# Optimization experiments

Hardware: AMD Instinct MI355X
Metric: run time of the kernel (lower is better)

## Reference

```python
import jax, jax.numpy as jnp
import numpy as np

B, S, D = 2, 2048, 4096
H, KVH, HD = 32, 8, 128
MULT = 0.08838834764831845  # 1/sqrt(head_dim)
MAXV = 30.0                 # tanh soft-cap
ROPE_BASE = 10000.0


def _rope_cos_sin(position_ids, hd=HD, base=ROPE_BASE):
    inv_freq = 1.0 / (base ** (jnp.arange(0, hd, 2, dtype=jnp.float32) / hd))
    freqs = position_ids.astype(jnp.float32)[..., None] * inv_freq  # [B,S,hd/2]
    emb = jnp.concatenate([freqs, freqs], axis=-1)                  # [B,S,hd]
    return jnp.cos(emb), jnp.sin(emb)


def _rotate_half(x):
    half = x.shape[-1] // 2
    return jnp.concatenate([-x[..., half:], x[..., :half]], axis=-1)


def setup_inputs() -> dict:
    key = jax.random.key(0)
    ks = jax.random.split(key, 5)
    hidden_states = jax.random.normal(ks[0], (B, S, D), dtype=jnp.float32)
    position_ids = jnp.broadcast_to(jnp.arange(S, dtype=jnp.int64), (B, S))
    # True = masked (causal upper triangle)
    causal = jnp.triu(jnp.ones((S, S), dtype=bool), k=1)
    attention_mask = jnp.broadcast_to(causal, (B, 1, S, S))
    sc = 0.02
    q_w = jax.random.normal(ks[1], (D, H * HD), dtype=jnp.float32) * sc
    k_w = jax.random.normal(ks[2], (D, KVH * HD), dtype=jnp.float32) * sc
    v_w = jax.random.normal(ks[3], (D, KVH * HD), dtype=jnp.float32) * sc
    o_w = jax.random.normal(ks[4], (H * HD, D), dtype=jnp.float32) * sc
    return {"hidden_states": hidden_states, "position_ids": position_ids,
            "attention_mask": attention_mask, "q_w": q_w, "k_w": k_w,
            "v_w": v_w, "o_w": o_w}


def reference(hidden_states, position_ids, attention_mask, q_w, k_w, v_w, o_w):
    bsz, q_len, _ = hidden_states.shape
    q = (hidden_states @ q_w).reshape(bsz, q_len, H, HD).transpose(0, 2, 1, 3)    # [B,H,S,HD]
    k = (hidden_states @ k_w).reshape(bsz, q_len, KVH, HD).transpose(0, 2, 1, 3)  # [B,KVH,S,HD]
    v = (hidden_states @ v_w).reshape(bsz, q_len, KVH, HD).transpose(0, 2, 1, 3)

    cos, sin = _rope_cos_sin(position_ids)   # [B,S,HD]
    cos = cos[:, None]                       # [B,1,S,HD]
    sin = sin[:, None]
    q = q * cos + _rotate_half(q) * sin
    k = k * cos + _rotate_half(k) * sin

    groups = H // KVH
    k = jnp.repeat(k, groups, axis=1)        # [B,H,S,HD]
    v = jnp.repeat(v, groups, axis=1)

    scores = jnp.einsum('bhqd,bhkd->bhqk', q, k).astype(jnp.float32) * MULT
    scores = MAXV * jnp.tanh(scores / MAXV)
    scores = jnp.where(attention_mask, jnp.float32(-10000.0), scores)
    attn = jax.nn.softmax(scores, axis=-1).astype(q.dtype)

    out = jnp.einsum('bhqk,bhkd->bhqd', attn, v)       # [B,H,S,HD]
    out = out.transpose(0, 2, 1, 3).reshape(bsz, q_len, H * HD)
    return out @ o_w
```

## Files before the change

kernel.cpp:

```cpp
#include <hip/hip_runtime.h>
#include <stdint.h>

#define B_ 2
#define S_ 2048
#define D_ 4096
#define H_ 32
#define KVH_ 8
#define HD_ 128
#define GRP_ (H_/KVH_)
#define NQKV 6144
#define MULT_ 0.08838834764831845f
#define MAXV_ 30.0f

typedef __attribute__((ext_vector_type(8))) short s16x8;
typedef __attribute__((ext_vector_type(4))) float fx4;

__device__ __forceinline__ unsigned short f2bf(float f) {
  unsigned int u = __float_as_uint(f);
  u += 0x7fffu + ((u >> 16) & 1u);
  return (unsigned short)(u >> 16);
}
__device__ __forceinline__ float bf2f(unsigned short h) {
  return __uint_as_float(((unsigned int)h) << 16);
}

__device__ __forceinline__ void gld_lds16(const void* g, void* l) {
  __builtin_amdgcn_global_load_lds(
      (const __attribute__((address_space(1))) unsigned int*)g,
      (__attribute__((address_space(3))) unsigned int*)l, 16, 0, 0);
}


__global__ void k_f2bf(const float* __restrict__ src, unsigned short* __restrict__ dst, int n4) {
  int i = blockIdx.x * blockDim.x + threadIdx.x;
  int stride = gridDim.x * blockDim.x;
  for (; i < n4; i += stride) {
    float4 v = ((const float4*)src)[i];
    ushort4 o;
    o.x = f2bf(v.x); o.y = f2bf(v.y); o.z = f2bf(v.z); o.w = f2bf(v.w);
    ((ushort4*)dst)[i] = o;
  }
}

__global__ void k_transpose_w(const float* __restrict__ src, int ncols,
                              unsigned short* __restrict__ dst) {
  __shared__ float tile[32][33];
  int k0 = blockIdx.x * 32;
  int n0 = blockIdx.y * 32;
  int tx = threadIdx.x, ty = threadIdx.y;
  for (int i = 0; i < 32; i += 8)
    tile[ty + i][tx] = src[(size_t)(k0 + ty + i) * ncols + n0 + tx];
  __syncthreads();
  for (int i = 0; i < 32; i += 8)
    dst[(size_t)(n0 + ty + i) * 4096 + k0 + tx] = f2bf(tile[tx][ty + i]);
}

__global__ void k_transpose_v(const unsigned short* __restrict__ qkv,
                              unsigned short* __restrict__ vt) {
  __shared__ unsigned short tile[32][33];
  int s0 = blockIdx.x * 32;
  int d0 = blockIdx.y * 32;
  int bk = blockIdx.z;
  int b = bk / KVH_, kvh = bk % KVH_;
  int tx = threadIdx.x, ty = threadIdx.y;
  for (int i = 0; i < 32; i += 8)
    tile[ty + i][tx] = qkv[(size_t)(b*S_ + s0 + ty + i)*NQKV + 5120 + kvh*HD_ + d0 + tx];
  __syncthreads();
  for (int i = 0; i < 32; i += 8)
    vt[((size_t)bk*HD_ + d0 + ty + i)*S_ + s0 + tx] = tile[tx][ty + i];
}

__global__ void k_rope(const unsigned short* __restrict__ qkv,
                       unsigned short* __restrict__ Q, unsigned short* __restrict__ K) {
  int bs = blockIdx.x;
  int b = bs >> 11;
  int s = bs & (S_ - 1);
  __shared__ float cs[64], sn[64];
  int t = threadIdx.x;
  if (t < 64) {
    float inv = __expf(-(float)t * 0.14391156831212787f);
    float fr = (float)s * inv;
    cs[t] = cosf(fr); sn[t] = sinf(fr);
  }
  __syncthreads();
  const unsigned short* row = qkv + (size_t)bs * NQKV;
  for (int i = t; i < H_*HD_; i += 256) {
    int h = i >> 7, d = i & 127;
    float x = bf2f(row[i]);
    float x2, c, si;
    if (d < 64) { x2 = -bf2f(row[h*128 + d + 64]); c = cs[d];    si = sn[d]; }
    else        { x2 =  bf2f(row[h*128 + d - 64]); c = cs[d-64]; si = sn[d-64]; }
    Q[((size_t)(b*H_ + h)*S_ + s)*HD_ + d] = f2bf(x*c + x2*si);
  }
  for (int i = t; i < KVH_*HD_; i += 256) {
    int h = i >> 7, d = i & 127;
    float x = bf2f(row[4096 + i]);
    float x2, c, si;
    if (d < 64) { x2 = -bf2f(row[4096 + h*128 + d + 64]); c = cs[d];    si = sn[d]; }
    else        { x2 =  bf2f(row[4096 + h*128 + d - 64]); c = cs[d-64]; si = sn[d-64]; }
    K[((size_t)(b*KVH_ + h)*S_ + s)*HD_ + d] = f2bf(x*c + x2*si);
  }
}


#define BAR() asm volatile("s_barrier" ::: "memory")
#define SB0() __builtin_amdgcn_sched_barrier(0)

#define STAGE(buf, isB, h, kt) do {                                          \
  const unsigned short* _src = (isB) ? Bt : A;                               \
  size_t _rb = (size_t)(((isB) ? bn : bm)*((isB) ? BN : 256)                 \
                        + (h)*((isB) ? BN/2 : 128));                         \
  _Pragma("unroll") for (int _rr = 0; _rr < ((isB) ? BN/128 : 2); ++_rr) {   \
    int _s = _rr*8 + wv;                                                     \
    gld_lds16(_src + (_rb + (size_t)((_s>>1)*16))*Kd                         \
                   + (size_t)((kt)*64 + (_s&1)*32) + lane_off,               \
              ldsc + (buf)*PBUF + (isB)*32768                                \
                   + (h)*((isB) ? BN*64 : 16384) + _s*1024);                 \
  }                                                                          \
} while (0)

#define LDA(dst, buf, mh) do {                                               \
  _Pragma("unroll") for (int _i = 0; _i < 4; ++_i)                           \
  _Pragma("unroll") for (int _kk = 0; _kk < 2; ++_kk)                        \
    dst[_i*2+_kk] = *(const s16x8*)(ldsc + (buf)*PBUF + wr*16384             \
                    + ((((mh)*4+_i)*2+_kk)*1024) + aswz);                    \
} while (0)

#define LDB(dst, buf, nh) do {                                               \
  _Pragma("unroll") for (int _j = 0; _j < NFR; ++_j)                         \
  _Pragma("unroll") for (int _kk = 0; _kk < 2; ++_kk)                        \
    dst[_j*2+_kk] = *(const s16x8*)(ldsc + (buf)*PBUF + 32768                \
                    + (wc>>1)*(BN*64)                                        \
                    + ((((wc&1)*2*NFR+(nh)*NFR+_j)*2+_kk)*1024) + aswz);     \
} while (0)

#define MFMA_Q(Aa, Bb, MH, NH) do {                                          \
  __builtin_amdgcn_s_setprio(1);                                            \
  _Pragma("unroll") for (int _i = 0; _i < 4; ++_i)                           \
  _Pragma("unroll") for (int _j = 0; _j < NFR; ++_j)                         \
  _Pragma("unroll") for (int _kk = 0; _kk < 2; ++_kk)                        \
    acc[(MH)*4+_i][(NH)*NFR+_j] = __builtin_amdgcn_mfma_f32_16x16x32_bf16(   \
        Aa[_i*2+_kk], Bb[_j*2+_kk], acc[(MH)*4+_i][(NH)*NFR+_j], 0, 0, 0);   \
  __builtin_amdgcn_s_setprio(0);                                            \
} while (0)

template<int OUTF32, int BN>
__global__ __launch_bounds__(512, 2)
void k_gemm8(const unsigned short* __restrict__ A, const unsigned short* __restrict__ Bt,
             void* __restrict__ C, int Kdim, int N, int MB) {
  constexpr int NFR = BN / 128;
  constexpr int PBUF = 32768 + BN * 128;
  __shared__ __align__(16) char ldsbuf[2 * PBUF];
  char* ldsc = ldsbuf;
  const size_t Kd = (size_t)Kdim;
  const int NT = Kdim >> 6;

  auto VMCN = [] {
    if constexpr (BN == 256) asm volatile("s_waitcnt vmcnt(4)" ::: "memory");
    else                     asm volatile("s_waitcnt vmcnt(2)" ::: "memory");
  };

  int nwg = gridDim.x;
  int flat = blockIdx.x;
  int q = nwg >> 3, r8 = nwg & 7, xcd = flat & 7, off = flat >> 3;
  int wg = (xcd < r8 ? xcd*(q+1) : r8*(q+1) + (xcd-r8)*q) + off;
  int bm = wg % MB, bn = wg / MB;

  int tid = threadIdx.x;
  int lane = tid & 63, wv = tid >> 6;
  int wr = wv >> 2, wc = wv & 3;
  int l15 = lane & 15, l4 = lane >> 4;
  const int aswz = (l15 << 6) + ((l4 << 4) ^ ((l15 & 8) ? 32 : 0));
  const size_t lane_off = (size_t)(lane >> 2) * Kd
                        + (size_t)(((lane & 3) << 3) ^ ((lane & 32) >> 1));

  fx4 acc[8][2*NFR] = {};
  s16x8 Afr[8], B0fr[2*NFR], B1fr[2*NFR];

  STAGE(0, 0, 0, 0); STAGE(0, 0, 1, 0);
  STAGE(0, 1, 0, 0); STAGE(0, 1, 1, 0);
  STAGE(1, 1, 0, 1); STAGE(1, 1, 1, 1);
  VMCN();
  BAR();

  for (int t2 = 0; t2 < NT; t2 += 2) {
    int tb1 = t2 + 1;
    int tn0 = t2 + 2; if (tn0 >= NT) tn0 -= NT;
    int tn1 = t2 + 3; if (tn1 >= NT) tn1 -= NT;
    LDA(Afr, 0, 0); LDB(B0fr, 0, 0);
    STAGE(1, 0, 0, tb1);
    BAR();
    MFMA_Q(Afr, B0fr, 0, 0);
    SB0(); BAR();
    LDB(B1fr, 0, 1);
    STAGE(1, 0, 1, tb1);
    BAR();
    MFMA_Q(Afr, B1fr, 0, 1);
    SB0(); BAR();
    LDA(Afr, 0, 1);
    STAGE(0, 1, 0, tn0);
    BAR();
    MFMA_Q(Afr, B1fr, 1, 1);
    SB0(); BAR();
    STAGE(0, 1, 1, tn0);
    BAR();
    MFMA_Q(Afr, B0fr, 1, 0);
    SB0(); VMCN(); BAR();
    LDA(Afr, 1, 0); LDB(B0fr, 1, 0);
    STAGE(0, 0, 0, tn0);
    BAR();
    MFMA_Q(Afr, B0fr, 0, 0);
    SB0(); BAR();
    LDB(B1fr, 1, 1);
    STAGE(0, 0, 1, tn0);
    BAR();
    MFMA_Q(Afr, B1fr, 0, 1);
    SB0(); BAR();
    LDA(Afr, 1, 1);
    STAGE(1, 1, 0, tn1);
    BAR();
    MFMA_Q(Afr, B1fr, 1, 1);
    SB0(); BAR();
    STAGE(1, 1, 1, tn1);
    BAR();
    MFMA_Q(Afr, B0fr, 1, 0);
    SB0(); VMCN(); BAR();
  }

  int m0 = bm*256 + wr*128 + l4*4;
#pragma unroll
  for (int mf = 0; mf < 8; ++mf)
#pragma unroll
    for (int nf = 0; nf < 2*NFR; ++nf)
#pragma unroll
      for (int r = 0; r < 4; ++r) {
        int m = m0 + mf*16 + r;
        int n = bn*BN + (wc>>1)*(BN/2) + ((wc&1)*2*NFR + nf)*16 + l15;
        float v = acc[mf][nf][r];
        if (OUTF32) ((float*)C)[(size_t)m*N + n] = v;
        else ((unsigned short*)C)[(size_t)m*N + n] = f2bf(v);
      }
}


__global__ __launch_bounds__(256)
void k_attn7(const unsigned short* __restrict__ Q, const unsigned short* __restrict__ K,
             const unsigned short* __restrict__ Vt, unsigned short* __restrict__ Aout) {
  __shared__ unsigned short k_lds[2][32*128];
  __shared__ unsigned short v_lds[2][128*32];
  const float C1 = 0.08838834764831845f * 2.0f * 1.4426950408889634f / 30.0f;
  const float C2 = 30.0f * 1.4426950408889634f;
  int strip = 15 - blockIdx.x;
  int bh = blockIdx.y;
  int b = bh >> 5, h = bh & 31;
  int kvh = h >> 2;
  int tid = threadIdx.x, lane = tid & 63, wv = tid >> 6;
  int l15 = lane & 15, l4 = lane >> 4;
  const unsigned short* Qb = Q + (size_t)bh * S_ * HD_;
  const unsigned short* Kb = K + (size_t)(b*KVH_ + kvh) * S_ * HD_;
  const unsigned short* Vb = Vt + (size_t)(b*KVH_ + kvh) * HD_ * S_;

  int q0 = strip * 128;
  int qbase = q0 + wv * 32;
  s16x8 bq[2][4];
#pragma unroll
  for (int qf = 0; qf < 2; ++qf)
#pragma unroll
    for (int kb = 0; kb < 4; ++kb)
      bq[qf][kb] = *(const s16x8*)&Qb[(size_t)(qbase + qf*16 + l15)*HD_ + kb*32 + l4*8];

  s16x8 ones;
#pragma unroll
  for (int i = 0; i < 8; ++i) ones[i] = (short)0x3F80;

  fx4 oacc[2][8] = {};
  fx4 osum[2] = {};

  int nt_full = qbase >> 5;
  int nt_blk = strip*4 + 4;

#define STAGE_KV32(bufi, kb32) do {                                          \
  _Pragma("unroll") for (int _it = 0; _it < 2; ++_it) {                      \
    int _c = _it*256 + tid;                                                  \
    int _kr = _c >> 4;                                                       \
    int _kd = ((_c & 15) ^ (_kr & 7)) * 8;                                   \
    gld_lds16(&Kb[(size_t)((kb32) + _kr)*HD_ + _kd],                         \
              &k_lds[bufi][_it*2048 + wv*512]);                              \
    int _vd = _c >> 2;                                                       \
    int _vk = ((_c & 3) ^ (_vd & 3)) * 8;                                    \
    gld_lds16(&Vb[(size_t)_vd*S_ + (kb32) + _vk],                            \
              &v_lds[bufi][_it*2048 + wv*512]);                              \
  }                                                                          \
} while (0)

  auto body = [&](int bufi, int kbase, bool domask) {
    fx4 sst[2][2] = {};
    __builtin_amdgcn_s_setprio(1);
#pragma unroll
    for (int nb = 0; nb < 2; ++nb)
#pragma unroll
      for (int kb = 0; kb < 4; ++kb) {
        s16x8 kf = *(const s16x8*)&k_lds[bufi][(nb*16 + l15)*128 + (((kb*4 + l4) ^ (l15 & 7)) * 8)];
        sst[nb][0] = __builtin_amdgcn_mfma_f32_16x16x32_bf16(kf, bq[0][kb], sst[nb][0], 0, 0, 0);
        sst[nb][1] = __builtin_amdgcn_mfma_f32_16x16x32_bf16(kf, bq[1][kb], sst[nb][1], 0, 0, 0);
      }
    __builtin_amdgcn_s_setprio(0);
    s16x8 pf[2];
#pragma unroll
    for (int qf = 0; qf < 2; ++qf) {
      int qr = qbase + qf*16 + l15;
      uint32_t w[4];
#pragma unroll
      for (int nb = 0; nb < 2; ++nb) {
        float pv[4];
#pragma unroll
        for (int r = 0; r < 4; ++r) {
          float sraw = sst[nb][qf][r];
          float e2 = __builtin_amdgcn_exp2f(-fabsf(sraw) * C1);
          float th = (1.f - e2) * __builtin_amdgcn_rcpf(1.f + e2);
          float th_s = __uint_as_float(__float_as_uint(th) |
                                       (__float_as_uint(sraw) & 0x80000000u));
          float p = __builtin_amdgcn_exp2f(th_s * C2 - C2);
          if (domask) {
            int kk = kbase + nb*16 + l4*4 + r;
            p = (kk <= qr) ? p : 0.f;
          }
          pv[r] = p;
        }
        w[nb*2]   = __builtin_amdgcn_perm(__float_as_uint(pv[1]), __float_as_uint(pv[0]), 0x07060302u);
        w[nb*2+1] = __builtin_amdgcn_perm(__float_as_uint(pv[3]), __float_as_uint(pv[2]), 0x07060302u);
      }
      uint32_t a0x = __shfl_xor((int)w[0], 16), a1x = __shfl_xor((int)w[1], 16);
      uint32_t b0x = __shfl_xor((int)w[2], 16), b1x = __shfl_xor((int)w[3], 16);
      bool up = (l4 & 1);
      uint32_t VA0 = up ? a0x : w[0], VA1 = up ? a1x : w[1];
      uint32_t VA2 = up ? w[0] : a0x, VA3 = up ? w[1] : a1x;
      uint32_t VB0 = up ? b0x : w[2], VB1 = up ? b1x : w[3];
      uint32_t VB2 = up ? w[2] : b0x, VB3 = up ? w[3] : b1x;
      bool lowh = (l4 < 2);
      uint32_t X0 = lowh ? VB0 : VA0, X1 = lowh ? VB1 : VA1;
      uint32_t X2 = lowh ? VB2 : VA2, X3 = lowh ? VB3 : VA3;
      uint32_t Y0 = __shfl_xor((int)X0, 32), Y1 = __shfl_xor((int)X1, 32);
      uint32_t Y2 = __shfl_xor((int)X2, 32), Y3 = __shfl_xor((int)X3, 32);
      union { uint32_t u[4]; s16x8 v; } tw;
      tw.u[0] = (l4 == 0) ? VA0 : (l4 == 3) ? VB0 : Y0;
      tw.u[1] = (l4 == 0) ? VA1 : (l4 == 3) ? VB1 : Y1;
      tw.u[2] = (l4 == 0) ? VA2 : (l4 == 3) ? VB2 : Y2;
      tw.u[3] = (l4 == 0) ? VA3 : (l4 == 3) ? VB3 : Y3;
      pf[qf] = tw.v;
    }
    __builtin_amdgcn_s_setprio(1);
    osum[0] = __builtin_amdgcn_mfma_f32_16x16x32_bf16(ones, pf[0], osum[0], 0, 0, 0);
    osum[1] = __builtin_amdgcn_mfma_f32_16x16x32_bf16(ones, pf[1], osum[1], 0, 0, 0);
#pragma unroll
    for (int db = 0; db < 8; ++db) {
      int d = db*16 + l15;
      s16x8 vf = *(const s16x8*)&v_lds[bufi][d*32 + ((l4 ^ (d & 3)) * 8)];
      oacc[0][db] = __builtin_amdgcn_mfma_f32_16x16x32_bf16(vf, pf[0], oacc[0][db], 0, 0, 0);
      oacc[1][db] = __builtin_amdgcn_mfma_f32_16x16x32_bf16(vf, pf[1], oacc[1][db], 0, 0, 0);
    }
    __builtin_amdgcn_s_setprio(0);
  };

  STAGE_KV32(0, 0);
  __syncthreads();
  for (int t = 0; t < nt_blk; ++t) {
    int bufi = t & 1;
    int kbase = t*32;
    if (t + 1 < nt_blk) STAGE_KV32(bufi^1, (t+1)*32);
    if (t < nt_full)       body(bufi, kbase, false);
    else if (t == nt_full) body(bufi, kbase, true);
    __syncthreads();
  }
#undef STAGE_KV32

#pragma unroll
  for (int qf = 0; qf < 2; ++qf) {
    float rn = __builtin_amdgcn_rcpf(osum[qf][0]);
    int qq = qbase + qf*16 + l15;
#pragma unroll
    for (int db = 0; db < 8; ++db) {
      ushort4 o;
      o.x = f2bf(oacc[qf][db][0] * rn);
      o.y = f2bf(oacc[qf][db][1] * rn);
      o.z = f2bf(oacc[qf][db][2] * rn);
      o.w = f2bf(oacc[qf][db][3] * rn);
      *(ushort4*)&Aout[(size_t)(b*S_ + qq)*4096 + h*HD_ + db*16 + l4*4] = o;
    }
  }
}


extern "C" void kernel_launch(void* const* d_in, const int* in_sizes, int n_in,
                              void* d_out, int out_size, void* d_ws, size_t ws_size,
                              hipStream_t stream) {
  (void)in_sizes; (void)n_in; (void)out_size; (void)ws_size;
  const float* hidden = (const float*)d_in[0];
  const float* q_w = (const float*)d_in[3];
  const float* k_w = (const float*)d_in[4];
  const float* v_w = (const float*)d_in[5];
  const float* o_w = (const float*)d_in[6];
  char* ws = (char*)d_ws;
  unsigned short* hidden_bf = (unsigned short*)(ws + 0);
  unsigned short* qkv_wt    = (unsigned short*)(ws + 33554432);
  unsigned short* o_wt      = (unsigned short*)(ws + 83886080);
  unsigned short* qkv       = (unsigned short*)(ws + 117440512);
  unsigned short* Qb        = (unsigned short*)(ws + 167772160);
  unsigned short* Kb        = (unsigned short*)(ws + 201326592);
  unsigned short* Vt        = (unsigned short*)(ws + 209715200);
  unsigned short* attn_out  = (unsigned short*)(ws + 218103808);

  dim3 tb(32, 8);
  k_f2bf<<<2048, 256, 0, stream>>>(hidden, hidden_bf, (B_*S_*D_)/4);
  k_transpose_w<<<dim3(128, 128), tb, 0, stream>>>(q_w, 4096, qkv_wt);
  k_transpose_w<<<dim3(128, 32),  tb, 0, stream>>>(k_w, 1024, qkv_wt + (size_t)4096*4096);
  k_transpose_w<<<dim3(128, 32),  tb, 0, stream>>>(v_w, 1024, qkv_wt + (size_t)5120*4096);
  k_transpose_w<<<dim3(128, 128), tb, 0, stream>>>(o_w, 4096, o_wt);
  k_gemm8<0,128><<<dim3(16*48), 512, 0, stream>>>(hidden_bf, qkv_wt, qkv, D_, NQKV, 16);
  k_rope<<<B_*S_, 256, 0, stream>>>(qkv, Qb, Kb);
  k_transpose_v<<<dim3(S_/32, HD_/32, B_*KVH_), tb, 0, stream>>>(qkv, Vt);
  k_attn7<<<dim3(16, 64), 256, 0, stream>>>(Qb, Kb, Vt, attn_out);
  k_gemm8<1,256><<<dim3(16*16), 512, 0, stream>>>(attn_out, o_wt, d_out, D_, D_, 16);
}
```

Before: 662.5 us.

## Pair short and long causal query strips per block and simplify tanh-softmax math

```diff
diff --git a/kernel.cpp b/kernel.cpp
--- a/kernel.cpp
+++ b/kernel.cpp
@@ -244,13 +244,13 @@
 
 
 __global__ __launch_bounds__(256)
-void k_attn7(const unsigned short* __restrict__ Q, const unsigned short* __restrict__ K,
+void k_attn8(const unsigned short* __restrict__ Q, const unsigned short* __restrict__ K,
              const unsigned short* __restrict__ Vt, unsigned short* __restrict__ Aout) {
   __shared__ unsigned short k_lds[2][32*128];
   __shared__ unsigned short v_lds[2][128*32];
-  const float C1 = 0.08838834764831845f * 2.0f * 1.4426950408889634f / 30.0f;
-  const float C2 = 30.0f * 1.4426950408889634f;
-  int strip = 15 - blockIdx.x;
+  const float C1 = MULT_ * 2.0f * 1.4426950408889634f / MAXV_;
+  const float C3 = 2.0f * MAXV_ * 1.4426950408889634f;
+  int tpair = blockIdx.x;
   int bh = blockIdx.y;
   int b = bh >> 5, h = bh & 31;
   int kvh = h >> 2;
@@ -260,24 +260,9 @@
   const unsigned short* Kb = K + (size_t)(b*KVH_ + kvh) * S_ * HD_;
   const unsigned short* Vb = Vt + (size_t)(b*KVH_ + kvh) * HD_ * S_;
 
-  int q0 = strip * 128;
-  int qbase = q0 + wv * 32;
-  s16x8 bq[2][4];
-#pragma unroll
-  for (int qf = 0; qf < 2; ++qf)
-#pragma unroll
-    for (int kb = 0; kb < 4; ++kb)
-      bq[qf][kb] = *(const s16x8*)&Qb[(size_t)(qbase + qf*16 + l15)*HD_ + kb*32 + l4*8];
-
   s16x8 ones;
 #pragma unroll
   for (int i = 0; i < 8; ++i) ones[i] = (short)0x3F80;
-
-  fx4 oacc[2][8] = {};
-  fx4 osum[2] = {};
-
-  int nt_full = qbase >> 5;
-  int nt_blk = strip*4 + 4;
 
 #define STAGE_KV32(bufi, kb32) do {                                          \
   _Pragma("unroll") for (int _it = 0; _it < 2; ++_it) {                      \
@@ -293,34 +278,40 @@
   }                                                                          \
 } while (0)
 
-  auto body = [&](int bufi, int kbase, bool domask) {
-    fx4 sst[2][2] = {};
-    __builtin_amdgcn_s_setprio(1);
-#pragma unroll
-    for (int nb = 0; nb < 2; ++nb)
-#pragma unroll
-      for (int kb = 0; kb < 4; ++kb) {
-        s16x8 kf = *(const s16x8*)&k_lds[bufi][(nb*16 + l15)*128 + (((kb*4 + l4) ^ (l15 & 7)) * 8)];
-        sst[nb][0] = __builtin_amdgcn_mfma_f32_16x16x32_bf16(kf, bq[0][kb], sst[nb][0], 0, 0, 0);
-        sst[nb][1] = __builtin_amdgcn_mfma_f32_16x16x32_bf16(kf, bq[1][kb], sst[nb][1], 0, 0, 0);
-      }
-    __builtin_amdgcn_s_setprio(0);
-    s16x8 pf[2];
-#pragma unroll
-    for (int qf = 0; qf < 2; ++qf) {
-      int qr = qbase + qf*16 + l15;
+  for (int sp = 0; sp < 2; ++sp) {
+    int strip = sp ? (31 - tpair) : tpair;
+    int q0 = strip * 64;
+    int qbase = q0 + wv * 16;
+    int qr = qbase + l15;
+    s16x8 bq[4];
+#pragma unroll
+    for (int kb = 0; kb < 4; ++kb)
+      bq[kb] = *(const s16x8*)&Qb[(size_t)qr*HD_ + kb*32 + l4*8];
+    fx4 oacc[8] = {};
+    fx4 osum = {};
+    int nt_full = qbase >> 5;
+    int nt = (q0 >> 5) + 2;
+
+    auto body = [&](int bufi, int kbase, bool domask) {
+      fx4 sst[2] = {};
+      __builtin_amdgcn_s_setprio(1);
+#pragma unroll
+      for (int nb = 0; nb < 2; ++nb)
+#pragma unroll
+        for (int kb = 0; kb < 4; ++kb) {
+          s16x8 kf = *(const s16x8*)&k_lds[bufi][(nb*16 + l15)*128 + (((kb*4 + l4) ^ (l15 & 7)) * 8)];
+          sst[nb] = __builtin_amdgcn_mfma_f32_16x16x32_bf16(kf, bq[kb], sst[nb], 0, 0, 0);
+        }
+      __builtin_amdgcn_s_setprio(0);
       uint32_t w[4];
 #pragma unroll
       for (int nb = 0; nb < 2; ++nb) {
         float pv[4];
 #pragma unroll
         for (int r = 0; r < 4; ++r) {
-          float sraw = sst[nb][qf][r];
-          float e2 = __builtin_amdgcn_exp2f(-fabsf(sraw) * C1);
-          float th = (1.f - e2) * __builtin_amdgcn_rcpf(1.f + e2);
-          float th_s = __uint_as_float(__float_as_uint(th) |
-                                       (__float_as_uint(sraw) & 0x80000000u));
-          float p = __builtin_amdgcn_exp2f(th_s * C2 - C2);
+          float sraw = sst[nb][r];
+          float e2p = __builtin_amdgcn_exp2f(sraw * C1);
+          float p = __builtin_amdgcn_exp2f(-C3 * __builtin_amdgcn_rcpf(1.f + e2p));
           if (domask) {
             int kk = kbase + nb*16 + l4*4 + r;
             p = (kk <= qr) ? p : 0.f;
@@ -347,47 +338,40 @@
       tw.u[1] = (l4 == 0) ? VA1 : (l4 == 3) ? VB1 : Y1;
       tw.u[2] = (l4 == 0) ? VA2 : (l4 == 3) ? VB2 : Y2;
       tw.u[3] = (l4 == 0) ? VA3 : (l4 == 3) ? VB3 : Y3;
-      pf[qf] = tw.v;
+      s16x8 pf = tw.v;
+      __builtin_amdgcn_s_setprio(1);
+      osum = __builtin_amdgcn_mfma_f32_16x16x32_bf16(ones, pf, osum, 0, 0, 0);
+#pragma unroll
+      for (int db = 0; db < 8; ++db) {
+        int d = db*16 + l15;
+        s16x8 vf = *(const s16x8*)&v_lds[bufi][d*32 + ((l4 ^ (d & 3)) * 8)];
+        oacc[db] = __builtin_amdgcn_mfma_f32_16x16x32_bf16(vf, pf, oacc[db], 0, 0, 0);
+      }
+      __builtin_amdgcn_s_setprio(0);
+    };
+
+    STAGE_KV32(0, 0);
+    __syncthreads();
+    for (int t = 0; t < nt; ++t) {
+      int bufi = t & 1;
+      if (t + 1 < nt) STAGE_KV32(bufi^1, (t+1)*32);
+      if (t < nt_full)       body(bufi, t*32, false);
+      else if (t == nt_full) body(bufi, t*32, true);
+      __syncthreads();
     }
-    __builtin_amdgcn_s_setprio(1);
-    osum[0] = __builtin_amdgcn_mfma_f32_16x16x32_bf16(ones, pf[0], osum[0], 0, 0, 0);
-    osum[1] = __builtin_amdgcn_mfma_f32_16x16x32_bf16(ones, pf[1], osum[1], 0, 0, 0);
-#pragma unroll
-    for (int db = 0; db < 8; ++db) {
-      int d = db*16 + l15;
-      s16x8 vf = *(const s16x8*)&v_lds[bufi][d*32 + ((l4 ^ (d & 3)) * 8)];
-      oacc[0][db] = __builtin_amdgcn_mfma_f32_16x16x32_bf16(vf, pf[0], oacc[0][db], 0, 0, 0);
-      oacc[1][db] = __builtin_amdgcn_mfma_f32_16x16x32_bf16(vf, pf[1], oacc[1][db], 0, 0, 0);
-    }
-    __builtin_amdgcn_s_setprio(0);
-  };
-
-  STAGE_KV32(0, 0);
-  __syncthreads();
-  for (int t = 0; t < nt_blk; ++t) {
-    int bufi = t & 1;
-    int kbase = t*32;
-    if (t + 1 < nt_blk) STAGE_KV32(bufi^1, (t+1)*32);
-    if (t < nt_full)       body(bufi, kbase, false);
-    else if (t == nt_full) body(bufi, kbase, true);
-    __syncthreads();
-  }
-#undef STAGE_KV32
-
-#pragma unroll
-  for (int qf = 0; qf < 2; ++qf) {
-    float rn = __builtin_amdgcn_rcpf(osum[qf][0]);
-    int qq = qbase + qf*16 + l15;
+
+    float rn = __builtin_amdgcn_rcpf(osum[0]);
 #pragma unroll
     for (int db = 0; db < 8; ++db) {
       ushort4 o;
-      o.x = f2bf(oacc[qf][db][0] * rn);
-      o.y = f2bf(oacc[qf][db][1] * rn);
-      o.z = f2bf(oacc[qf][db][2] * rn);
-      o.w = f2bf(oacc[qf][db][3] * rn);
-      *(ushort4*)&Aout[(size_t)(b*S_ + qq)*4096 + h*HD_ + db*16 + l4*4] = o;
+      o.x = f2bf(oacc[db][0] * rn);
+      o.y = f2bf(oacc[db][1] * rn);
+      o.z = f2bf(oacc[db][2] * rn);
+      o.w = f2bf(oacc[db][3] * rn);
+      *(ushort4*)&Aout[(size_t)(b*S_ + qr)*4096 + h*HD_ + db*16 + l4*4] = o;
     }
   }
+#undef STAGE_KV32
 }
 
 
@@ -419,6 +403,6 @@
   k_gemm8<0,128><<<dim3(16*48), 512, 0, stream>>>(hidden_bf, qkv_wt, qkv, D_, NQKV, 16);
   k_rope<<<B_*S_, 256, 0, stream>>>(qkv, Qb, Kb);
   k_transpose_v<<<dim3(S_/32, HD_/32, B_*KVH_), tb, 0, stream>>>(qkv, Vt);
-  k_attn7<<<dim3(16, 64), 256, 0, stream>>>(Qb, Kb, Vt, attn_out);
+  k_attn8<<<dim3(16, 64), 256, 0, stream>>>(Qb, Kb, Vt, attn_out);
   k_gemm8<1,256><<<dim3(16*16), 512, 0, stream>>>(attn_out, o_wt, d_out, D_, D_, 16);
 }
```

Result: faster. 586.7 us (-11.4%).
